# Optimization experiments

Hardware: AMD Instinct MI355X
Metric: run time of the kernel (lower is better)

## Reference

```python
import jax, jax.numpy as jnp
import numpy as np

NUM_ENT = 50000
NUM_REL2 = 474   # num_relations * 2
E = 400000
D = 100          # embedding / hidden dim (hardcoded in module)
B = 4            # num_bases
NEG_SLOPE = 0.2  # PyG RGATConv default


def setup_inputs() -> dict:
    key = jax.random.key(0)
    ks = jax.random.split(key, 8)
    inp = {
        "entity": jnp.arange(NUM_ENT, dtype=jnp.int32),
        "edge_index": jax.random.randint(ks[0], (2, E), 0, NUM_ENT),
        "edge_type": jax.random.randint(ks[1], (E,), 0, NUM_REL2),
        "edge_norm": jax.random.normal(ks[2], (E,), dtype=jnp.float32),
        "emb": jax.random.normal(ks[3], (NUM_ENT, D), dtype=jnp.float32),
    }
    scale = 1.0 / np.sqrt(D).astype(np.float32)
    for i, p in enumerate(("1", "2")):
        k = jax.random.split(ks[4 + i], 4)
        inp["basis" + p] = jax.random.normal(k[0], (B, D, D), dtype=jnp.float32) * scale
        inp["att" + p] = jax.random.normal(k[1], (NUM_REL2, B), dtype=jnp.float32) * 0.5
        inp["q" + p] = jax.random.normal(k[2], (D, 1), dtype=jnp.float32) * scale
        inp["k" + p] = jax.random.normal(k[3], (D, 1), dtype=jnp.float32) * scale
        inp["bias" + p] = jnp.zeros((D,), jnp.float32)
    return inp


def segment_softmax(scores, seg, num_segments):
    # numerically stable softmax over edges grouped by destination node
    m = jax.ops.segment_max(scores, seg, num_segments=num_segments)
    ex = jnp.exp(scores - m[seg])
    s = jax.ops.segment_sum(ex, seg, num_segments=num_segments)
    return ex / (s[seg] + 1e-16)


def rgat_conv(x, src, dst, etype, basis, att, q, k, bias, num_nodes):
    # basis decomposition: per-relation weight W_r = sum_b att[r,b] * basis[b]
    # computed implicitly: project x through each basis once, mix per-edge.
    xb = jnp.einsum('ni,bio->nbo', x, basis)          # [N, B, D]
    att_e = att[etype]                                # [E, B]
    hj = jnp.einsum('eb,ebo->eo', att_e, xb[src])     # transformed source feats [E, D]
    xq = jnp.einsum('nbo,oh->nb', xb, q)              # per-node, per-basis q-score [N, B]
    xk = jnp.einsum('nbo,oh->nb', xb, k)
    q_e = jnp.sum(att_e * xq[dst], axis=1)            # [E]
    k_e = jnp.sum(att_e * xk[src], axis=1)            # [E]
    alpha = jax.nn.leaky_relu(q_e + k_e, NEG_SLOPE)   # additive self-attention
    alpha = segment_softmax(alpha, dst, num_nodes)    # across-relation softmax per dst
    out = jax.ops.segment_sum(alpha[:, None] * hj, dst, num_segments=num_nodes)
    return out + bias


def reference(entity, edge_index, edge_type, edge_norm, emb,
              basis1, att1, q1, k1, bias1,
              basis2, att2, q2, k2, bias2):
    src, dst = edge_index[0], edge_index[1]
    n = entity.shape[0]
    x = emb[entity]                                   # [N, 100]
    x = jax.nn.relu(rgat_conv(x, src, dst, edge_type, basis1, att1, q1, k1, bias1, n))
    # dropout is identity in eval mode
    x = rgat_conv(x, src, dst, edge_type, basis2, att2, q2, k2, bias2, n)
    return x
```

## Files before the change

kernel.cpp:

```cpp
#include <hip/hip_runtime.h>

constexpr int N = 50000;
constexpr int E = 400000;
constexpr int D = 100;
constexpr int B = 4;
constexpr float NEG_SLOPE = 0.2f;

constexpr int SCAN_CHUNK = 2048;
constexpr int NB_SCAN = (N + SCAN_CHUNK - 1) / SCAN_CHUNK;
constexpr int CAP = 128;


__global__ void k_hist(const int* __restrict__ dst, int* __restrict__ deg) {
  int i = blockIdx.x * blockDim.x + threadIdx.x;
  int stride = gridDim.x * blockDim.x;
  for (; i < E; i += stride) atomicAdd(&deg[dst[i]], 1);
}

__global__ void k_scan1(const int* __restrict__ deg, int* __restrict__ incl,
                        int* __restrict__ bsums) {
  __shared__ int lds[256];
  int tid = threadIdx.x;
  int base = blockIdx.x * SCAN_CHUNK + tid * 8;
  int v[8]; int s = 0;
#pragma unroll
  for (int j = 0; j < 8; ++j) {
    int idx = base + j;
    int x = (idx < N) ? deg[idx] : 0;
    v[j] = x; s += x;
  }
  lds[tid] = s; __syncthreads();
  for (int off = 1; off < 256; off <<= 1) {
    int t = (tid >= off) ? lds[tid - off] : 0;
    __syncthreads();
    lds[tid] += t;
    __syncthreads();
  }
  int run = lds[tid] - s;
#pragma unroll
  for (int j = 0; j < 8; ++j) {
    int idx = base + j;
    run += v[j];
    if (idx < N) incl[idx] = run;
  }
  if (tid == 255) bsums[blockIdx.x] = lds[255];
}

__global__ void k_scan2(int* __restrict__ bsums, int nb) {
  if (threadIdx.x == 0 && blockIdx.x == 0) {
    int run = 0;
    for (int i = 0; i < nb; ++i) { int t = bsums[i]; bsums[i] = run; run += t; }
  }
}

__global__ void k_scan3(const int* __restrict__ incl, const int* __restrict__ bsums,
                        int* __restrict__ offs) {
  int i = blockIdx.x * blockDim.x + threadIdx.x;
  int stride = gridDim.x * blockDim.x;
  for (; i < N; i += stride) {
    offs[i + 1] = incl[i] + bsums[i / SCAN_CHUNK];
    if (i == 0) offs[0] = 0;
  }
}

__global__ void k_scatter(const int* __restrict__ srcArr, const int* __restrict__ dst,
                          const int* __restrict__ etype, const int* __restrict__ offs,
                          int* __restrict__ cursor, int* __restrict__ ssorted,
                          int* __restrict__ esorted) {
  int i = blockIdx.x * blockDim.x + threadIdx.x;
  int stride = gridDim.x * blockDim.x;
  for (; i < E; i += stride) {
    int d = dst[i];
    int pos = offs[d] + atomicAdd(&cursor[d], 1);
    ssorted[pos] = srcArr[i];
    esorted[pos] = etype[i];
  }
}

__global__ void k_gather(const float* __restrict__ emb, const int* __restrict__ entity,
                         float* __restrict__ X) {
  int idx = blockIdx.x * blockDim.x + threadIdx.x;
  int total = N * (D / 4);
  int stride = gridDim.x * blockDim.x;
  for (; idx < total; idx += stride) {
    int n = idx / (D / 4), c = idx % (D / 4);
    int r = entity[n];
    *(float4*)(X + (size_t)n * D + c * 4) = *(const float4*)(emb + (size_t)r * D + c * 4);
  }
}


__global__ void k_qbkb(const float* __restrict__ basis, const float* __restrict__ qv,
                       const float* __restrict__ kv, float* __restrict__ qb,
                       float* __restrict__ kb) {
  int t = blockIdx.x * blockDim.x + threadIdx.x;
  if (t < B * D) {
    const float* row = basis + t * D;
    float sq = 0.f, sk = 0.f;
    for (int o = 0; o < D; ++o) { float r = row[o]; sq += r * qv[o]; sk += r * kv[o]; }
    qb[t] = sq; kb[t] = sk;
  }
}

__global__ __launch_bounds__(256) void k_xqxk(
    const float* __restrict__ X, const float* __restrict__ qb,
    const float* __restrict__ kb, float* __restrict__ xq, float* __restrict__ xk) {
  __shared__ float qb_s[B * D], kb_s[B * D];
  int tid = threadIdx.x;
  for (int i = tid; i < B * D; i += 256) { qb_s[i] = qb[i]; kb_s[i] = kb[i]; }
  __syncthreads();
  int n = blockIdx.x * 256 + tid;
  if (n >= N) return;
  const float* x = X + (size_t)n * D;
  float aq[B] = {}, ak[B] = {};
  for (int i = 0; i < D; i += 4) {
    float4 xv = *(const float4*)(x + i);
#pragma unroll
    for (int b = 0; b < B; ++b) {
      float4 qv = *(const float4*)&qb_s[b * D + i];
      float4 kv = *(const float4*)&kb_s[b * D + i];
      aq[b] += xv.x * qv.x + xv.y * qv.y + xv.z * qv.z + xv.w * qv.w;
      ak[b] += xv.x * kv.x + xv.y * kv.y + xv.z * kv.z + xv.w * kv.w;
    }
  }
  *(float4*)(xq + (size_t)n * 4) = make_float4(aq[0], aq[1], aq[2], aq[3]);
  *(float4*)(xk + (size_t)n * 4) = make_float4(ak[0], ak[1], ak[2], ak[3]);
}

__device__ __forceinline__ float edge_score_p(int s, int et,
                                              const float* __restrict__ att,
                                              const float4 xq4,
                                              const float* __restrict__ xk,
                                              float4* a_out) {
  float4 a = *(const float4*)(att + et * 4);
  float4 xs = *(const float4*)(xk + s * 4);
  float qe = a.x * xq4.x + a.y * xq4.y + a.z * xq4.z + a.w * xq4.w;
  float ke = a.x * xs.x + a.y * xs.y + a.z * xs.z + a.w * xs.w;
  float sc = qe + ke;
  *a_out = a;
  return sc >= 0.f ? sc : NEG_SLOPE * sc;
}

__global__ __launch_bounds__(128) void k_node(
    const float* __restrict__ feat, const int* __restrict__ ssorted,
    const int* __restrict__ esorted, const float* __restrict__ att,
    const float* __restrict__ xq, const float* __restrict__ xk,
    const int* __restrict__ offs, float* __restrict__ agg) {
  int n = blockIdx.x;
  int tid = threadIdx.x;
  int lane = tid & 63, wid = tid >> 6;
  int o0 = offs[n], o1 = offs[n + 1];
  int deg = o1 - o0;
  float4 xq4 = *(const float4*)(xq + (size_t)n * 4);
  __shared__ float red[2];
  __shared__ float sc[CAP];
  __shared__ float4 a4[CAP];
  __shared__ int sbuf[CAP];

  if (deg <= CAP) {
    for (int i = tid; i < deg; i += 128) {
      int s = ssorted[o0 + i];
      int et = esorted[o0 + i];
      float4 a;
      float v = edge_score_p(s, et, att, xq4, xk, &a);
      sc[i] = v; a4[i] = a; sbuf[i] = s;
    }
    __syncthreads();
    float lm = -3.4e38f;
    for (int i = tid; i < deg; i += 128) lm = fmaxf(lm, sc[i]);
#pragma unroll
    for (int off = 32; off >= 1; off >>= 1) lm = fmaxf(lm, __shfl_xor(lm, off));
    if (lane == 0) red[wid] = lm;
    __syncthreads();
    float m = fmaxf(red[0], red[1]);
    __syncthreads();
    float ls = 0.f;
    for (int i = tid; i < deg; i += 128) {
      float ex = __expf(sc[i] - m);
      sc[i] = ex;
      ls += ex;
    }
#pragma unroll
    for (int off = 32; off >= 1; off >>= 1) ls += __shfl_xor(ls, off);
    if (lane == 0) red[wid] = ls;
    __syncthreads();
    float inv = 1.f / (red[0] + red[1] + 1e-16f);
    for (int i = tid; i < deg; i += 128) {
      float p = sc[i] * inv;
      float4 a = a4[i];
      a.x *= p; a.y *= p; a.z *= p; a.w *= p;
      a4[i] = a;
    }
    __syncthreads();
    if (tid < D) {
      float acc0 = 0.f, acc1 = 0.f, acc2 = 0.f, acc3 = 0.f;
      int i = 0;
      for (; i + 1 < deg; i += 2) {
        float4 aA = a4[i];     int sA = sbuf[i];
        float4 aB = a4[i + 1]; int sB = sbuf[i + 1];
        float xA = feat[(size_t)sA * D + tid];
        float xB = feat[(size_t)sB * D + tid];
        acc0 += aA.x * xA + aB.x * xB;
        acc1 += aA.y * xA + aB.y * xB;
        acc2 += aA.z * xA + aB.z * xB;
        acc3 += aA.w * xA + aB.w * xB;
      }
      if (i < deg) {
        float4 a = a4[i]; int s = sbuf[i];
        float xv = feat[(size_t)s * D + tid];
        acc0 += a.x * xv; acc1 += a.y * xv; acc2 += a.z * xv; acc3 += a.w * xv;
      }
      float* ag = agg + (size_t)n * (B * D) + tid;
      ag[0 * D] = acc0; ag[1 * D] = acc1; ag[2 * D] = acc2; ag[3 * D] = acc3;
    }
  } else {
    float lm = -3.4e38f;
    for (int i = tid; i < deg; i += 128) {
      float4 a;
      lm = fmaxf(lm, edge_score_p(ssorted[o0 + i], esorted[o0 + i], att, xq4, xk, &a));
    }
#pragma unroll
    for (int off = 32; off >= 1; off >>= 1) lm = fmaxf(lm, __shfl_xor(lm, off));
    if (lane == 0) red[wid] = lm;
    __syncthreads();
    float m = fmaxf(red[0], red[1]);
    __syncthreads();
    float ls = 0.f;
    for (int i = tid; i < deg; i += 128) {
      float4 a;
      ls += __expf(edge_score_p(ssorted[o0 + i], esorted[o0 + i], att, xq4, xk, &a) - m);
    }
#pragma unroll
    for (int off = 32; off >= 1; off >>= 1) ls += __shfl_xor(ls, off);
    if (lane == 0) red[wid] = ls;
    __syncthreads();
    float inv = 1.f / (red[0] + red[1] + 1e-16f);
    if (tid < D) {
      float acc0 = 0.f, acc1 = 0.f, acc2 = 0.f, acc3 = 0.f;
      for (int i = 0; i < deg; ++i) {
        int s = ssorted[o0 + i];
        float4 a;
        float v = edge_score_p(s, esorted[o0 + i], att, xq4, xk, &a);
        float p = __expf(v - m) * inv;
        float xv = feat[(size_t)s * D + tid];
        acc0 += p * a.x * xv;
        acc1 += p * a.y * xv;
        acc2 += p * a.z * xv;
        acc3 += p * a.w * xv;
      }
      float* ag = agg + (size_t)n * (B * D) + tid;
      ag[0 * D] = acc0; ag[1 * D] = acc1; ag[2 * D] = acc2; ag[3 * D] = acc3;
    }
  }
}

template <bool RELU>
__global__ __launch_bounds__(256) void k_gemm(const float* __restrict__ A,
                                              const float* __restrict__ W,
                                              const float* __restrict__ bias,
                                              float* __restrict__ out) {
  __shared__ float A_lds[64][36];
  __shared__ float W_lds[32][128];
  int tid = threadIdx.x;
  int nblk = blockIdx.x * 64;
  int o_lo = (tid & 15) * 4;
  int n_base = (tid >> 4) * 4;
  float acc[4][8] = {};
  for (int kc = 0; kc < 400; kc += 32) {
#pragma unroll
    for (int j = 0; j < 2; ++j) {
      int idx = tid + j * 256;
      int n_l = idx >> 3;
      int k4 = (idx & 7) * 4;
      int gn = nblk + n_l;
      float4 av = make_float4(0.f, 0.f, 0.f, 0.f);
      if (gn < N && kc + k4 + 3 < 400) av = *(const float4*)(A + (size_t)gn * 400 + kc + k4);
      *(float4*)&A_lds[n_l][k4] = av;
    }
#pragma unroll
    for (int j = 0; j < 4; ++j) {
      int idx = tid + j * 256;
      int k = idx >> 5;
      int o4 = (idx & 31) * 4;
      float4 v = make_float4(0.f, 0.f, 0.f, 0.f);
      if (o4 < D && kc + k < 400) v = *(const float4*)(W + (size_t)(kc + k) * D + o4);
      *(float4*)&W_lds[k][o4] = v;
    }
    __syncthreads();
#pragma unroll 4
    for (int k = 0; k < 32; ++k) {
      float4 w0 = *(const float4*)&W_lds[k][o_lo];
      float4 w1 = *(const float4*)&W_lds[k][o_lo + 64];
      float w[8] = {w0.x, w0.y, w0.z, w0.w, w1.x, w1.y, w1.z, w1.w};
#pragma unroll
      for (int i = 0; i < 4; ++i) {
        float a = A_lds[n_base + i][k];
#pragma unroll
        for (int jj = 0; jj < 8; ++jj) acc[i][jj] += a * w[jj];
      }
    }
    __syncthreads();
  }
  bool hi_ok = (o_lo + 64 < D - 3);
  float4 b0 = *(const float4*)(bias + o_lo);
  float4 b1 = hi_ok ? *(const float4*)(bias + o_lo + 64) : make_float4(0, 0, 0, 0);
#pragma unroll
  for (int i = 0; i < 4; ++i) {
    int gn = nblk + n_base + i;
    if (gn < N) {
      float4 r0, r1;
      r0.x = acc[i][0] + b0.x; r0.y = acc[i][1] + b0.y;
      r0.z = acc[i][2] + b0.z; r0.w = acc[i][3] + b0.w;
      r1.x = acc[i][4] + b1.x; r1.y = acc[i][5] + b1.y;
      r1.z = acc[i][6] + b1.z; r1.w = acc[i][7] + b1.w;
      if (RELU) {
        r0.x = fmaxf(r0.x, 0.f); r0.y = fmaxf(r0.y, 0.f);
        r0.z = fmaxf(r0.z, 0.f); r0.w = fmaxf(r0.w, 0.f);
        r1.x = fmaxf(r1.x, 0.f); r1.y = fmaxf(r1.y, 0.f);
        r1.z = fmaxf(r1.z, 0.f); r1.w = fmaxf(r1.w, 0.f);
      }
      *(float4*)(out + (size_t)gn * D + o_lo) = r0;
      if (hi_ok) *(float4*)(out + (size_t)gn * D + o_lo + 64) = r1;
    }
  }
}


extern "C" void kernel_launch(void* const* d_in, const int* in_sizes, int n_in,
                              void* d_out, int out_size, void* d_ws, size_t ws_size,
                              hipStream_t stream) {
  const int* entity = (const int*)d_in[0];
  const int* edge_index = (const int*)d_in[1];
  const int* etype = (const int*)d_in[2];
  const float* emb = (const float*)d_in[4];
  const float* basis1 = (const float*)d_in[5];
  const float* att1 = (const float*)d_in[6];
  const float* q1 = (const float*)d_in[7];
  const float* k1 = (const float*)d_in[8];
  const float* bias1 = (const float*)d_in[9];
  const float* basis2 = (const float*)d_in[10];
  const float* att2 = (const float*)d_in[11];
  const float* q2 = (const float*)d_in[12];
  const float* k2 = (const float*)d_in[13];
  const float* bias2 = (const float*)d_in[14];
  float* out = (float*)d_out;

  const int* srcArr = edge_index;
  const int* dstArr = edge_index + E;

  float* ws = (float*)d_ws;
  float* agg = ws;
  float* X1 = agg + (size_t)N * B * D;
  float* xq = X1 + (size_t)N * D;
  float* xk = xq + (size_t)N * B;
  float* qb = xk + (size_t)N * B;
  float* kb = qb + B * D;
  int* ssorted = (int*)(kb + B * D);
  int* esorted = ssorted + E;
  int* offs = esorted + E;
  int* deg = offs + (N + 1);
  int* cursor = deg + N;
  int* incl = cursor + N;
  int* bsums = incl + N;

  hipMemsetAsync(deg, 0, N * sizeof(int), stream);
  hipMemsetAsync(cursor, 0, N * sizeof(int), stream);
  k_hist<<<512, 256, 0, stream>>>(dstArr, deg);
  k_scan1<<<NB_SCAN, 256, 0, stream>>>(deg, incl, bsums);
  k_scan2<<<1, 64, 0, stream>>>(bsums, NB_SCAN);
  k_scan3<<<256, 256, 0, stream>>>(incl, bsums, offs);
  k_scatter<<<512, 256, 0, stream>>>(srcArr, dstArr, etype, offs, cursor, ssorted, esorted);
  k_gather<<<1024, 256, 0, stream>>>(emb, entity, X1);

  k_qbkb<<<2, 256, 0, stream>>>(basis1, q1, k1, qb, kb);
  k_xqxk<<<(N + 255) / 256, 256, 0, stream>>>(X1, qb, kb, xq, xk);
  k_node<<<N, 128, 0, stream>>>(X1, ssorted, esorted, att1, xq, xk, offs, agg);
  k_gemm<true><<<(N + 63) / 64, 256, 0, stream>>>(agg, basis1, bias1, out);

  k_qbkb<<<2, 256, 0, stream>>>(basis2, q2, k2, qb, kb);
  k_xqxk<<<(N + 255) / 256, 256, 0, stream>>>(out, qb, kb, xq, xk);
  k_node<<<N, 128, 0, stream>>>(out, ssorted, esorted, att2, xq, xk, offs, agg);
  k_gemm<false><<<(N + 63) / 64, 256, 0, stream>>>(agg, basis2, bias2, out);
}
```

Baseline: 484.6 us.

## Replace fp32 SIMT basis GEMM with split-bf16 MFMA GEMM

The node aggregation kernel now writes its per-basis aggregates as hi/lo bf16 pairs, and the final projection uses a new MFMA kernel doing three bf16 16x16x32 products per tile to approximate fp32 accuracy. Transposed, padded hi/lo copies of both basis weight sets are prepared once per call. This aims to move the dense N×400×100 GEMM onto matrix cores instead of scalar FMA loops. The trade-off is slightly reduced precision from dropping the lo×lo term, plus an extra small weight-prep kernel.

New measurement: 444.7 us. 8.2% less time.

```diff
diff --git a/kernel.cpp b/kernel.cpp
--- a/kernel.cpp
+++ b/kernel.cpp
@@ -1,6 +1,7 @@
 #include <hip/hip_runtime.h>
 
 constexpr int N = 50000;
+constexpr int NPAD = 50048;
 constexpr int E = 400000;
 constexpr int D = 100;
 constexpr int B = 4;
@@ -9,6 +10,18 @@
 constexpr int SCAN_CHUNK = 2048;
 constexpr int NB_SCAN = (N + SCAN_CHUNK - 1) / SCAN_CHUNK;
 constexpr int CAP = 128;
+
+typedef __attribute__((ext_vector_type(8))) short short8v;
+typedef __attribute__((ext_vector_type(4))) float f32x4;
+
+__device__ __forceinline__ unsigned short f2bf(float f) {
+  unsigned int u = __float_as_uint(f);
+  unsigned int r = u + 0x7FFFu + ((u >> 16) & 1u);
+  return (unsigned short)(r >> 16);
+}
+__device__ __forceinline__ float bf2f(unsigned short h) {
+  return __uint_as_float((unsigned int)h << 16);
+}
 
 
 __global__ void k_hist(const int* __restrict__ dst, int* __restrict__ deg) {
@@ -87,6 +100,21 @@
     int r = entity[n];
     *(float4*)(X + (size_t)n * D + c * 4) = *(const float4*)(emb + (size_t)r * D + c * 4);
   }
+}
+
+__global__ void k_wprep(const float* __restrict__ W1, const float* __restrict__ W2,
+                        unsigned short* __restrict__ h1, unsigned short* __restrict__ l1,
+                        unsigned short* __restrict__ h2, unsigned short* __restrict__ l2) {
+  int idx = blockIdx.x * blockDim.x + threadIdx.x;
+  if (idx >= 112 * 416) return;
+  int o = idx / 416, k = idx % 416;
+  bool ok = (o < D) && (k < 400);
+  float v1 = ok ? W1[k * D + o] : 0.f;
+  float v2 = ok ? W2[k * D + o] : 0.f;
+  unsigned short a = f2bf(v1);
+  h1[idx] = a; l1[idx] = f2bf(v1 - bf2f(a));
+  unsigned short b = f2bf(v2);
+  h2[idx] = b; l2[idx] = f2bf(v2 - bf2f(b));
 }
 
 
@@ -141,11 +169,20 @@
   return sc >= 0.f ? sc : NEG_SLOPE * sc;
 }
 
+__device__ __forceinline__ void write_bf_pair(unsigned short* __restrict__ Ahi,
+                                              unsigned short* __restrict__ Alo,
+                                              size_t idx, float v) {
+  unsigned short h = f2bf(v);
+  Ahi[idx] = h;
+  Alo[idx] = f2bf(v - bf2f(h));
+}
+
 __global__ __launch_bounds__(128) void k_node(
     const float* __restrict__ feat, const int* __restrict__ ssorted,
     const int* __restrict__ esorted, const float* __restrict__ att,
     const float* __restrict__ xq, const float* __restrict__ xk,
-    const int* __restrict__ offs, float* __restrict__ agg) {
+    const int* __restrict__ offs, unsigned short* __restrict__ Ahi,
+    unsigned short* __restrict__ Alo) {
   int n = blockIdx.x;
   int tid = threadIdx.x;
   int lane = tid & 63, wid = tid >> 6;
@@ -210,8 +247,11 @@
         float xv = feat[(size_t)s * D + tid];
         acc0 += a.x * xv; acc1 += a.y * xv; acc2 += a.z * xv; acc3 += a.w * xv;
       }
-      float* ag = agg + (size_t)n * (B * D) + tid;
-      ag[0 * D] = acc0; ag[1 * D] = acc1; ag[2 * D] = acc2; ag[3 * D] = acc3;
+      size_t base = (size_t)n * 400 + tid;
+      write_bf_pair(Ahi, Alo, base + 0 * D, acc0);
+      write_bf_pair(Ahi, Alo, base + 1 * D, acc1);
+      write_bf_pair(Ahi, Alo, base + 2 * D, acc2);
+      write_bf_pair(Ahi, Alo, base + 3 * D, acc3);
     }
   } else {
     float lm = -3.4e38f;
@@ -248,79 +288,67 @@
         acc2 += p * a.z * xv;
         acc3 += p * a.w * xv;
       }
-      float* ag = agg + (size_t)n * (B * D) + tid;
-      ag[0 * D] = acc0; ag[1 * D] = acc1; ag[2 * D] = acc2; ag[3 * D] = acc3;
-    }
-  }
-}
-
-template <bool RELU>
-__global__ __launch_bounds__(256) void k_gemm(const float* __restrict__ A,
-                                              const float* __restrict__ W,
-                                              const float* __restrict__ bias,
-                                              float* __restrict__ out) {
-  __shared__ float A_lds[64][36];
-  __shared__ float W_lds[32][128];
+      size_t base = (size_t)n * 400 + tid;
+      write_bf_pair(Ahi, Alo, base + 0 * D, acc0);
+      write_bf_pair(Ahi, Alo, base + 1 * D, acc1);
+      write_bf_pair(Ahi, Alo, base + 2 * D, acc2);
+      write_bf_pair(Ahi, Alo, base + 3 * D, acc3);
+    }
+  }
+}
+
+__global__ __launch_bounds__(256) void k_mfma(
+    const unsigned short* __restrict__ Ahi, const unsigned short* __restrict__ Alo,
+    const unsigned short* __restrict__ Wth, const unsigned short* __restrict__ Wtl,
+    const float* __restrict__ bias, float* __restrict__ out, int relu) {
   int tid = threadIdx.x;
-  int nblk = blockIdx.x * 64;
-  int o_lo = (tid & 15) * 4;
-  int n_base = (tid >> 4) * 4;
-  float acc[4][8] = {};
+  int lane = tid & 63;
+  int wv = tid >> 6;
+  int nbase = blockIdx.x * 64 + wv * 16;
+  int r16 = lane & 15;
+  int kgrp = lane >> 4;
+  f32x4 acc[7];
+#pragma unroll
+  for (int t = 0; t < 7; ++t) acc[t] = (f32x4){0.f, 0.f, 0.f, 0.f};
+
+  const unsigned short* arow_hi = Ahi + (size_t)(nbase + r16) * 400;
+  const unsigned short* arow_lo = Alo + (size_t)(nbase + r16) * 400;
+
+#pragma unroll 1
   for (int kc = 0; kc < 400; kc += 32) {
-#pragma unroll
-    for (int j = 0; j < 2; ++j) {
-      int idx = tid + j * 256;
-      int n_l = idx >> 3;
-      int k4 = (idx & 7) * 4;
-      int gn = nblk + n_l;
-      float4 av = make_float4(0.f, 0.f, 0.f, 0.f);
-      if (gn < N && kc + k4 + 3 < 400) av = *(const float4*)(A + (size_t)gn * 400 + kc + k4);
-      *(float4*)&A_lds[n_l][k4] = av;
-    }
-#pragma unroll
-    for (int j = 0; j < 4; ++j) {
-      int idx = tid + j * 256;
-      int k = idx >> 5;
-      int o4 = (idx & 31) * 4;
-      float4 v = make_float4(0.f, 0.f, 0.f, 0.f);
-      if (o4 < D && kc + k < 400) v = *(const float4*)(W + (size_t)(kc + k) * D + o4);
-      *(float4*)&W_lds[k][o4] = v;
-    }
-    __syncthreads();
-#pragma unroll 4
-    for (int k = 0; k < 32; ++k) {
-      float4 w0 = *(const float4*)&W_lds[k][o_lo];
-      float4 w1 = *(const float4*)&W_lds[k][o_lo + 64];
-      float w[8] = {w0.x, w0.y, w0.z, w0.w, w1.x, w1.y, w1.z, w1.w};
-#pragma unroll
-      for (int i = 0; i < 4; ++i) {
-        float a = A_lds[n_base + i][k];
-#pragma unroll
-        for (int jj = 0; jj < 8; ++jj) acc[i][jj] += a * w[jj];
+    int kofs = kc + kgrp * 8;
+    short8v ah, al;
+    if (kofs < 400) {
+      ah = *(const short8v*)(arow_hi + kofs);
+      al = *(const short8v*)(arow_lo + kofs);
+    } else {
+      ah = (short8v){0, 0, 0, 0, 0, 0, 0, 0};
+      al = ah;
+    }
+#pragma unroll
+    for (int t = 0; t < 7; ++t) {
+      size_t wb = (size_t)(t * 16 + r16) * 416 + kofs;
+      short8v bh = *(const short8v*)(Wth + wb);
+      short8v bl = *(const short8v*)(Wtl + wb);
+      acc[t] = __builtin_amdgcn_mfma_f32_16x16x32_bf16(ah, bh, acc[t], 0, 0, 0);
+      acc[t] = __builtin_amdgcn_mfma_f32_16x16x32_bf16(al, bh, acc[t], 0, 0, 0);
+      acc[t] = __builtin_amdgcn_mfma_f32_16x16x32_bf16(ah, bl, acc[t], 0, 0, 0);
+    }
+  }
+#pragma unroll
+  for (int t = 0; t < 7; ++t) {
+    int o = t * 16 + r16;
+    if (o < D) {
+      float bv = bias[o];
+#pragma unroll
+      for (int r = 0; r < 4; ++r) {
+        int gn = nbase + kgrp * 4 + r;
+        if (gn < N) {
+          float v = acc[t][r] + bv;
+          if (relu) v = fmaxf(v, 0.f);
+          out[(size_t)gn * D + o] = v;
+        }
       }
-    }
-    __syncthreads();
-  }
-  bool hi_ok = (o_lo + 64 < D - 3);
-  float4 b0 = *(const float4*)(bias + o_lo);
-  float4 b1 = hi_ok ? *(const float4*)(bias + o_lo + 64) : make_float4(0, 0, 0, 0);
-#pragma unroll
-  for (int i = 0; i < 4; ++i) {
-    int gn = nblk + n_base + i;
-    if (gn < N) {
-      float4 r0, r1;
-      r0.x = acc[i][0] + b0.x; r0.y = acc[i][1] + b0.y;
-      r0.z = acc[i][2] + b0.z; r0.w = acc[i][3] + b0.w;
-      r1.x = acc[i][4] + b1.x; r1.y = acc[i][5] + b1.y;
-      r1.z = acc[i][6] + b1.z; r1.w = acc[i][7] + b1.w;
-      if (RELU) {
-        r0.x = fmaxf(r0.x, 0.f); r0.y = fmaxf(r0.y, 0.f);
-        r0.z = fmaxf(r0.z, 0.f); r0.w = fmaxf(r0.w, 0.f);
-        r1.x = fmaxf(r1.x, 0.f); r1.y = fmaxf(r1.y, 0.f);
-        r1.z = fmaxf(r1.z, 0.f); r1.w = fmaxf(r1.w, 0.f);
-      }
-      *(float4*)(out + (size_t)gn * D + o_lo) = r0;
-      if (hi_ok) *(float4*)(out + (size_t)gn * D + o_lo + 64) = r1;
     }
   }
 }
@@ -348,14 +376,18 @@
   const int* srcArr = edge_index;
   const int* dstArr = edge_index + E;
 
-  float* ws = (float*)d_ws;
-  float* agg = ws;
-  float* X1 = agg + (size_t)N * B * D;
+  unsigned short* Ahi = (unsigned short*)d_ws;
+  unsigned short* Alo = Ahi + (size_t)NPAD * 400;
+  float* X1 = (float*)(Alo + (size_t)NPAD * 400);
   float* xq = X1 + (size_t)N * D;
   float* xk = xq + (size_t)N * B;
   float* qb = xk + (size_t)N * B;
   float* kb = qb + B * D;
-  int* ssorted = (int*)(kb + B * D);
+  unsigned short* Wth1 = (unsigned short*)(kb + B * D);
+  unsigned short* Wtl1 = Wth1 + 112 * 416;
+  unsigned short* Wth2 = Wtl1 + 112 * 416;
+  unsigned short* Wtl2 = Wth2 + 112 * 416;
+  int* ssorted = (int*)(Wtl2 + 112 * 416);
   int* esorted = ssorted + E;
   int* offs = esorted + E;
   int* deg = offs + (N + 1);
@@ -371,14 +403,15 @@
   k_scan3<<<256, 256, 0, stream>>>(incl, bsums, offs);
   k_scatter<<<512, 256, 0, stream>>>(srcArr, dstArr, etype, offs, cursor, ssorted, esorted);
   k_gather<<<1024, 256, 0, stream>>>(emb, entity, X1);
+  k_wprep<<<(112 * 416 + 255) / 256, 256, 0, stream>>>(basis1, basis2, Wth1, Wtl1, Wth2, Wtl2);
 
   k_qbkb<<<2, 256, 0, stream>>>(basis1, q1, k1, qb, kb);
   k_xqxk<<<(N + 255) / 256, 256, 0, stream>>>(X1, qb, kb, xq, xk);
-  k_node<<<N, 128, 0, stream>>>(X1, ssorted, esorted, att1, xq, xk, offs, agg);
-  k_gemm<true><<<(N + 63) / 64, 256, 0, stream>>>(agg, basis1, bias1, out);
+  k_node<<<N, 128, 0, stream>>>(X1, ssorted, esorted, att1, xq, xk, offs, Ahi, Alo);
+  k_mfma<<<NPAD / 64, 256, 0, stream>>>(Ahi, Alo, Wth1, Wtl1, bias1, out, 1);
 
   k_qbkb<<<2, 256, 0, stream>>>(basis2, q2, k2, qb, kb);
   k_xqxk<<<(N + 255) / 256, 256, 0, stream>>>(out, qb, kb, xq, xk);
-  k_node<<<N, 128, 0, stream>>>(out, ssorted, esorted, att2, xq, xk, offs, agg);
-  k_gemm<false><<<(N + 63) / 64, 256, 0, stream>>>(agg, basis2, bias2, out);
-}
+  k_node<<<N, 128, 0, stream>>>(out, ssorted, esorted, att2, xq, xk, offs, Ahi, Alo);
+  k_mfma<<<NPAD / 64, 256, 0, stream>>>(Ahi, Alo, Wth2, Wtl2, bias2, out, 0);
+}
```
